# Kernel optimization log

Hardware: AMD Instinct MI355X
Metric: run time of the kernel (lower is better)

The kernel has to match this reference:

```python
import jax, jax.numpy as jnp
import numpy as np

B, N, D, A = 128, 512, 300, 32


def setup_inputs() -> dict:
    key = jax.random.key(0)
    k1, k2, k3, k4 = jax.random.split(key, 4)
    node_reprs = jax.random.normal(k1, (B, N, D), dtype=jnp.float32)
    adjacency_matrices = (jax.random.uniform(k2, (B, N, N)) < 0.1).astype(jnp.float32)
    Wq = jax.random.normal(k3, (D, A), dtype=jnp.float32) * 0.01
    Wk = jax.random.normal(k4, (D, A), dtype=jnp.float32) * 0.01
    return {"node_reprs": node_reprs, "adjacency_matrices": adjacency_matrices,
            "Wq": Wq, "Wk": Wk}


def reference(node_reprs, adjacency_matrices, Wq, Wk):
    # Q = X Wq, K = X Wk  -> [B, N, A]
    Q = jnp.einsum('bnd,da->bna', node_reprs, Wq)
    K = jnp.einsum('bmd,da->bma', node_reprs, Wk)
    # scores elementwise-weighted by adjacency (NOT -inf masking), per original
    QK = jnp.einsum('bna,bma->bnm', Q, K) * adjacency_matrices
    attn = jax.nn.softmax(QK, axis=-1)  # torch softmax(dim=1) on [N,N] = last dim
    # aggregate node representations: [B, N, N] @ [B, N, D]
    return jnp.einsum('bnm,bmd->bnd', attn, node_reprs)
```

## Files before the change

### kernel.cpp

```cpp
#include <hip/hip_runtime.h>
#include <math.h>

constexpr int Bq = 128;
constexpr int Nn = 512;
constexpr int Dd = 300;
constexpr int Aa = 32;
constexpr int DT = 304;

typedef __attribute__((ext_vector_type(8))) short short8;
typedef __attribute__((ext_vector_type(4))) float float4v;

static __device__ __forceinline__ ushort f2bf(float x) {
    unsigned u = __float_as_uint(x);
    return (ushort)((u + 0x7FFF + ((u >> 16) & 1)) >> 16);
}

constexpr int KB_ROWS = 128;
constexpr int DCHUNK = 100;
constexpr int XS_STRIDE = 102;

__global__ __launch_bounds__(256) void proj_qk(
    const float* __restrict__ X, const float* __restrict__ Wq,
    const float* __restrict__ Wk, ushort* __restrict__ Qo, ushort* __restrict__ Ko,
    ushort* __restrict__ XbfT)
{
    __shared__ float xs[KB_ROWS * XS_STRIDE];
    const int b  = blockIdx.y;
    const int n0 = blockIdx.x * KB_ROWS;
    const int t  = threadIdx.x;
    const int c  = t & 15;
    const int r  = t >> 4;
    const int a4 = c * 4;
    const int rbase = r * 8;
    const float* Wbase = (a4 < Aa) ? (Wq + a4) : (Wk + (a4 - Aa));
    const float* Xb = X + ((size_t)(b * Nn + n0)) * Dd;

    float4 acc[8];
#pragma unroll
    for (int j = 0; j < 8; ++j) acc[j] = make_float4(0.f, 0.f, 0.f, 0.f);

    for (int d0 = 0; d0 < Dd; d0 += DCHUNK) {
        for (int l = t; l < KB_ROWS * (DCHUNK / 2); l += 256) {
            int row = l / (DCHUNK / 2);
            int dd2 = l - row * (DCHUNK / 2);
            *(float2*)(xs + row * XS_STRIDE + dd2 * 2) =
                *(const float2*)(Xb + (size_t)row * Dd + d0 + dd2 * 2);
        }
        __syncthreads();
        for (int dd = 0; dd < DCHUNK; ++dd) {
            float4 w4 = *(const float4*)(Wbase + (size_t)(d0 + dd) * Aa);
#pragma unroll
            for (int j = 0; j < 8; ++j) {
                float xv = xs[(rbase + j) * XS_STRIDE + dd];
                acc[j].x += xv * w4.x; acc[j].y += xv * w4.y;
                acc[j].z += xv * w4.z; acc[j].w += xv * w4.w;
            }
        }
        for (int l = t; l < KB_ROWS * DCHUNK; l += 256) {
            int dd  = l >> 7;
            int row = l & 127;
            XbfT[((size_t)b * DT + d0 + dd) * Nn + n0 + row] =
                f2bf(xs[row * XS_STRIDE + dd]);
        }
        __syncthreads();
    }

    ushort* Obase = (a4 < Aa) ? (Qo + a4) : (Ko + (a4 - Aa));
#pragma unroll
    for (int j = 0; j < 8; ++j) {
        int n = n0 + rbase + j;
        ushort4 o;
        o.x = f2bf(acc[j].x); o.y = f2bf(acc[j].y);
        o.z = f2bf(acc[j].z); o.w = f2bf(acc[j].w);
        *(ushort4*)(Obase + (size_t)(b * Nn + n) * Aa) = o;
    }
}

constexpr int TN = 32;

__global__ __launch_bounds__(256, 2) void attn_kernel(
    const float* __restrict__ Adj, const ushort* __restrict__ Qbf,
    const ushort* __restrict__ Kbf, const ushort* __restrict__ XbfT,
    float* __restrict__ Out)
{
    __shared__ __align__(16) ushort fragA[2 * 8192];
    __shared__ __align__(16) float wsum[4][TN];

    const int blk  = blockIdx.x;
    const int b    = ((blk >> 7) << 3) | (blk & 7);
    const int n0   = ((blk >> 3) & 15) * TN;

    const int t    = threadIdx.x;
    const int lane = t & 63;
    const int wv   = t >> 6;
    const int dl   = lane & 15;
    const int quad = lane >> 4;

    short8 qfr[2];
#pragma unroll
    for (int rs = 0; rs < 2; ++rs)
        qfr[rs] = *(const short8*)(Qbf + ((size_t)(b * Nn + n0 + rs * 16 + dl)) * Aa + quad * 8);

    const ushort* Kb    = Kbf + (size_t)b * Nn * Aa + (size_t)dl * Aa + quad * 8;
    const float*  arow0 = Adj + ((size_t)b * Nn + n0 + dl) * Nn + quad * 4;

    float dsum[2] = {0.f, 0.f};
    ushort* wpb = fragA + (quad >> 1) * 128 + dl * 8 + (quad & 1) * 4;

#pragma unroll
    for (int i = 0; i < 4; ++i) {
        const int ks = wv + i * 4;
        const int m0 = ks * 32;
        short8 kf0 = *(const short8*)(Kb + (size_t)m0 * Aa);
        short8 kf1 = *(const short8*)(Kb + (size_t)(m0 + 16) * Aa);
        ushort* wp = wpb + ks * 512;
#pragma unroll
        for (int rs = 0; rs < 2; ++rs) {
            const float* ar = arow0 + (size_t)rs * 16 * Nn + m0;
            float4 a0 = *(const float4*)(ar);
            float4 a1 = *(const float4*)(ar + 16);
            float4v z = {0.f, 0.f, 0.f, 0.f};
            float4v s0 = __builtin_amdgcn_mfma_f32_16x16x32_bf16(kf0, qfr[rs], z, 0, 0, 0);
            float4v s1 = __builtin_amdgcn_mfma_f32_16x16x32_bf16(kf1, qfr[rs], z, 0, 0, 0);
            float e0 = (a0.x != 0.f) ? __expf(s0[0]) : 1.0f;
            float e1 = (a0.y != 0.f) ? __expf(s0[1]) : 1.0f;
            float e2 = (a0.z != 0.f) ? __expf(s0[2]) : 1.0f;
            float e3 = (a0.w != 0.f) ? __expf(s0[3]) : 1.0f;
            float e4 = (a1.x != 0.f) ? __expf(s1[0]) : 1.0f;
            float e5 = (a1.y != 0.f) ? __expf(s1[1]) : 1.0f;
            float e6 = (a1.z != 0.f) ? __expf(s1[2]) : 1.0f;
            float e7 = (a1.w != 0.f) ? __expf(s1[3]) : 1.0f;
            dsum[rs] += ((e0 + e1) + (e2 + e3)) + ((e4 + e5) + (e6 + e7));
            uint2 w0, w1;
            w0.x = (unsigned)f2bf(e0) | ((unsigned)f2bf(e1) << 16);
            w0.y = (unsigned)f2bf(e2) | ((unsigned)f2bf(e3) << 16);
            w1.x = (unsigned)f2bf(e4) | ((unsigned)f2bf(e5) << 16);
            w1.y = (unsigned)f2bf(e6) | ((unsigned)f2bf(e7) << 16);
            *(uint2*)(wp + rs * 8192)       = w0;
            *(uint2*)(wp + rs * 8192 + 256) = w1;
        }
    }

#pragma unroll
    for (int rs = 0; rs < 2; ++rs) {
        float v = dsum[rs];
        v += __shfl_xor(v, 16);
        v += __shfl_xor(v, 32);
        if (lane < 16) wsum[wv][rs * 16 + lane] = v;
    }
    __syncthreads();

    float invr0[4], invr1[4];
    {
        float4 s0 = *(const float4*)&wsum[0][quad * 4];
        float4 s1 = *(const float4*)&wsum[0][16 + quad * 4];
#pragma unroll
        for (int w = 1; w < 4; ++w) {
            float4 t0 = *(const float4*)&wsum[w][quad * 4];
            float4 t1 = *(const float4*)&wsum[w][16 + quad * 4];
            s0.x += t0.x; s0.y += t0.y; s0.z += t0.z; s0.w += t0.w;
            s1.x += t1.x; s1.y += t1.y; s1.z += t1.z; s1.w += t1.w;
        }
        invr0[0] = 1.0f / s0.x; invr0[1] = 1.0f / s0.y;
        invr0[2] = 1.0f / s0.z; invr0[3] = 1.0f / s0.w;
        invr1[0] = 1.0f / s1.x; invr1[1] = 1.0f / s1.y;
        invr1[2] = 1.0f / s1.z; invr1[3] = 1.0f / s1.w;
    }

    const ushort* Xb  = XbfT + ((size_t)b * DT) * Nn;
    const ushort* afp = fragA + (size_t)lane * 8;

    for (int p = 0; p < 3; ++p) {
        const int dta = wv + p * 8;
        if (dta >= DT / 16) break;
        const int dtb = dta + 4;
        if (dtb < DT / 16) {
            const ushort* bba = Xb + (size_t)(dta * 16 + dl) * Nn + quad * 8;
            const ushort* bbb = Xb + (size_t)(dtb * 16 + dl) * Nn + quad * 8;
            float4v a0a = {0.f, 0.f, 0.f, 0.f};
            float4v a1a = {0.f, 0.f, 0.f, 0.f};
            float4v a0b = {0.f, 0.f, 0.f, 0.f};
            float4v a1b = {0.f, 0.f, 0.f, 0.f};
#pragma unroll
            for (int ks = 0; ks < 16; ++ks) {
                short8 bfa = *(const short8*)(bba + ks * 32);
                short8 bfb = *(const short8*)(bbb + ks * 32);
                short8 p0  = *(const short8*)(afp + ks * 512);
                short8 p1  = *(const short8*)(afp + 8192 + ks * 512);
                a0a = __builtin_amdgcn_mfma_f32_16x16x32_bf16(p0, bfa, a0a, 0, 0, 0);
                a1a = __builtin_amdgcn_mfma_f32_16x16x32_bf16(p1, bfa, a1a, 0, 0, 0);
                a0b = __builtin_amdgcn_mfma_f32_16x16x32_bf16(p0, bfb, a0b, 0, 0, 0);
                a1b = __builtin_amdgcn_mfma_f32_16x16x32_bf16(p1, bfb, a1b, 0, 0, 0);
            }
            const int da = dta * 16 + dl;
            const int db = dtb * 16 + dl;
#pragma unroll
            for (int r = 0; r < 4; ++r) {
                float* o0 = Out + ((size_t)(b * Nn + n0 + quad * 4 + r)) * Dd;
                float* o1 = Out + ((size_t)(b * Nn + n0 + 16 + quad * 4 + r)) * Dd;
                o0[da] = a0a[r] * invr0[r];
                o1[da] = a1a[r] * invr1[r];
                o0[db] = a0b[r] * invr0[r];
                o1[db] = a1b[r] * invr1[r];
            }
        } else {
            const ushort* bb = Xb + (size_t)(dta * 16 + dl) * Nn + quad * 8;
            float4v acc0 = {0.f, 0.f, 0.f, 0.f};
            float4v acc1 = {0.f, 0.f, 0.f, 0.f};
#pragma unroll
            for (int ks = 0; ks < 16; ++ks) {
                short8 bf = *(const short8*)(bb + ks * 32);
                short8 p0 = *(const short8*)(afp + ks * 512);
                short8 p1 = *(const short8*)(afp + 8192 + ks * 512);
                acc0 = __builtin_amdgcn_mfma_f32_16x16x32_bf16(p0, bf, acc0, 0, 0, 0);
                acc1 = __builtin_amdgcn_mfma_f32_16x16x32_bf16(p1, bf, acc1, 0, 0, 0);
            }
            const int d = dta * 16 + dl;
            if (d < Dd) {
#pragma unroll
                for (int r = 0; r < 4; ++r) {
                    Out[((size_t)(b * Nn + n0 + quad * 4 + r)) * Dd + d]      = acc0[r] * invr0[r];
                    Out[((size_t)(b * Nn + n0 + 16 + quad * 4 + r)) * Dd + d] = acc1[r] * invr1[r];
                }
            }
        }
    }
}

extern "C" void kernel_launch(void* const* d_in, const int* in_sizes, int n_in,
                              void* d_out, int out_size, void* d_ws, size_t ws_size,
                              hipStream_t stream) {
    const float* X   = (const float*)d_in[0];
    const float* Adj = (const float*)d_in[1];
    const float* Wq  = (const float*)d_in[2];
    const float* Wk  = (const float*)d_in[3];
    float* Out = (float*)d_out;

    ushort* Qbf  = (ushort*)d_ws;
    ushort* Kbf  = (ushort*)((char*)d_ws + (size_t)4 * 1024 * 1024);
    ushort* XbfT = (ushort*)((char*)d_ws + (size_t)8 * 1024 * 1024);

    proj_qk<<<dim3(Nn / KB_ROWS, Bq), 256, 0, stream>>>(X, Wq, Wk, Qbf, Kbf, XbfT);
    attn_kernel<<<dim3(Bq * Nn / TN), 256, 0, stream>>>(Adj, Qbf, Kbf, XbfT, Out);
}
```

Baseline: 407.2 us.

## Hoist K/adjacency loads and software-pipeline X fragment loads in aggregation loop

All K fragments and adjacency float4 values are loaded up front, before the score/exp loop, so their global latency overlaps instead of serializing per iteration. The aggregation phase is restructured so each wave handles five D-tiles in a single unrolled k-loop. X fragments are double-buffered two steps ahead, so MFMA work overlaps global loads. Wave 3 redundantly computes an extra tile (dt 15) that it discards, and register pressure rises from holding 16 float4 plus many short8 buffers, which may reduce occupancy.

```diff
diff --git a/kernel.cpp b/kernel.cpp
--- a/kernel.cpp
+++ b/kernel.cpp
@@ -104,24 +104,39 @@
     const ushort* Kb    = Kbf + (size_t)b * Nn * Aa + (size_t)dl * Aa + quad * 8;
     const float*  arow0 = Adj + ((size_t)b * Nn + n0 + dl) * Nn + quad * 4;
 
+    short8 kfr[8];
+#pragma unroll
+    for (int i = 0; i < 4; ++i) {
+        const int m0 = (wv + i * 4) * 32;
+        kfr[i * 2]     = *(const short8*)(Kb + (size_t)m0 * Aa);
+        kfr[i * 2 + 1] = *(const short8*)(Kb + (size_t)(m0 + 16) * Aa);
+    }
+    float4 ad[16];
+#pragma unroll
+    for (int i = 0; i < 4; ++i) {
+        const int m0 = (wv + i * 4) * 32;
+#pragma unroll
+        for (int rs = 0; rs < 2; ++rs) {
+            const float* ar = arow0 + (size_t)rs * 16 * Nn + m0;
+            ad[i * 4 + rs * 2]     = *(const float4*)(ar);
+            ad[i * 4 + rs * 2 + 1] = *(const float4*)(ar + 16);
+        }
+    }
+
     float dsum[2] = {0.f, 0.f};
     ushort* wpb = fragA + (quad >> 1) * 128 + dl * 8 + (quad & 1) * 4;
 
 #pragma unroll
     for (int i = 0; i < 4; ++i) {
         const int ks = wv + i * 4;
-        const int m0 = ks * 32;
-        short8 kf0 = *(const short8*)(Kb + (size_t)m0 * Aa);
-        short8 kf1 = *(const short8*)(Kb + (size_t)(m0 + 16) * Aa);
         ushort* wp = wpb + ks * 512;
 #pragma unroll
         for (int rs = 0; rs < 2; ++rs) {
-            const float* ar = arow0 + (size_t)rs * 16 * Nn + m0;
-            float4 a0 = *(const float4*)(ar);
-            float4 a1 = *(const float4*)(ar + 16);
+            float4 a0 = ad[i * 4 + rs * 2];
+            float4 a1 = ad[i * 4 + rs * 2 + 1];
             float4v z = {0.f, 0.f, 0.f, 0.f};
-            float4v s0 = __builtin_amdgcn_mfma_f32_16x16x32_bf16(kf0, qfr[rs], z, 0, 0, 0);
-            float4v s1 = __builtin_amdgcn_mfma_f32_16x16x32_bf16(kf1, qfr[rs], z, 0, 0, 0);
+            float4v s0 = __builtin_amdgcn_mfma_f32_16x16x32_bf16(kfr[i * 2],     qfr[rs], z, 0, 0, 0);
+            float4v s1 = __builtin_amdgcn_mfma_f32_16x16x32_bf16(kfr[i * 2 + 1], qfr[rs], z, 0, 0, 0);
             float e0 = (a0.x != 0.f) ? __expf(s0[0]) : 1.0f;
             float e1 = (a0.y != 0.f) ? __expf(s0[1]) : 1.0f;
             float e2 = (a0.z != 0.f) ? __expf(s0[2]) : 1.0f;
@@ -169,59 +184,59 @@
 
     const ushort* Xb  = XbfT + ((size_t)b * DT) * Nn;
     const ushort* afp = fragA + (size_t)lane * 8;
-
-    for (int p = 0; p < 3; ++p) {
-        const int dta = wv + p * 8;
-        if (dta >= DT / 16) break;
-        const int dtb = dta + 4;
-        if (dtb < DT / 16) {
-            const ushort* bba = Xb + (size_t)(dta * 16 + dl) * Nn + quad * 8;
-            const ushort* bbb = Xb + (size_t)(dtb * 16 + dl) * Nn + quad * 8;
-            float4v a0a = {0.f, 0.f, 0.f, 0.f};
-            float4v a1a = {0.f, 0.f, 0.f, 0.f};
-            float4v a0b = {0.f, 0.f, 0.f, 0.f};
-            float4v a1b = {0.f, 0.f, 0.f, 0.f};
-#pragma unroll
-            for (int ks = 0; ks < 16; ++ks) {
-                short8 bfa = *(const short8*)(bba + ks * 32);
-                short8 bfb = *(const short8*)(bbb + ks * 32);
-                short8 p0  = *(const short8*)(afp + ks * 512);
-                short8 p1  = *(const short8*)(afp + 8192 + ks * 512);
-                a0a = __builtin_amdgcn_mfma_f32_16x16x32_bf16(p0, bfa, a0a, 0, 0, 0);
-                a1a = __builtin_amdgcn_mfma_f32_16x16x32_bf16(p1, bfa, a1a, 0, 0, 0);
-                a0b = __builtin_amdgcn_mfma_f32_16x16x32_bf16(p0, bfb, a0b, 0, 0, 0);
-                a1b = __builtin_amdgcn_mfma_f32_16x16x32_bf16(p1, bfb, a1b, 0, 0, 0);
-            }
-            const int da = dta * 16 + dl;
-            const int db = dtb * 16 + dl;
+    const int dt4 = (wv < 3) ? (16 + wv) : 15;
+
+    const ushort* bp[5];
+#pragma unroll
+    for (int i = 0; i < 4; ++i)
+        bp[i] = Xb + (size_t)((wv + i * 4) * 16 + dl) * Nn + quad * 8;
+    bp[4] = Xb + (size_t)(dt4 * 16 + dl) * Nn + quad * 8;
+
+    float4v acc[5][2];
+#pragma unroll
+    for (int i = 0; i < 5; ++i) {
+        acc[i][0] = (float4v){0.f, 0.f, 0.f, 0.f};
+        acc[i][1] = (float4v){0.f, 0.f, 0.f, 0.f};
+    }
+
+    short8 xcur[5], xnxt[5];
+#pragma unroll
+    for (int i = 0; i < 5; ++i) xcur[i] = *(const short8*)(bp[i]);
+#pragma unroll
+    for (int i = 0; i < 5; ++i) xnxt[i] = *(const short8*)(bp[i] + 32);
+
+#pragma unroll
+    for (int ks = 0; ks < 16; ++ks) {
+        short8 p0 = *(const short8*)(afp + ks * 512);
+        short8 p1 = *(const short8*)(afp + 8192 + ks * 512);
+        short8 xc[5];
+#pragma unroll
+        for (int i = 0; i < 5; ++i) xc[i] = xcur[i];
+#pragma unroll
+        for (int i = 0; i < 5; ++i) xcur[i] = xnxt[i];
+        if (ks < 14) {
+#pragma unroll
+            for (int i = 0; i < 5; ++i) xnxt[i] = *(const short8*)(bp[i] + (ks + 2) * 32);
+        }
+#pragma unroll
+        for (int i = 0; i < 5; ++i) {
+            acc[i][0] = __builtin_amdgcn_mfma_f32_16x16x32_bf16(p0, xc[i], acc[i][0], 0, 0, 0);
+            acc[i][1] = __builtin_amdgcn_mfma_f32_16x16x32_bf16(p1, xc[i], acc[i][1], 0, 0, 0);
+        }
+    }
+
+#pragma unroll
+    for (int i = 0; i < 5; ++i) {
+        const int dt = (i < 4) ? (wv + i * 4) : dt4;
+        const int d  = dt * 16 + dl;
+        const bool ok = (i < 4) ? true : (wv < 3 && d < Dd);
+        if (ok) {
 #pragma unroll
             for (int r = 0; r < 4; ++r) {
                 float* o0 = Out + ((size_t)(b * Nn + n0 + quad * 4 + r)) * Dd;
                 float* o1 = Out + ((size_t)(b * Nn + n0 + 16 + quad * 4 + r)) * Dd;
-                o0[da] = a0a[r] * invr0[r];
-                o1[da] = a1a[r] * invr1[r];
-                o0[db] = a0b[r] * invr0[r];
-                o1[db] = a1b[r] * invr1[r];
-            }
-        } else {
-            const ushort* bb = Xb + (size_t)(dta * 16 + dl) * Nn + quad * 8;
-            float4v acc0 = {0.f, 0.f, 0.f, 0.f};
-            float4v acc1 = {0.f, 0.f, 0.f, 0.f};
-#pragma unroll
-            for (int ks = 0; ks < 16; ++ks) {
-                short8 bf = *(const short8*)(bb + ks * 32);
-                short8 p0 = *(const short8*)(afp + ks * 512);
-                short8 p1 = *(const short8*)(afp + 8192 + ks * 512);
-                acc0 = __builtin_amdgcn_mfma_f32_16x16x32_bf16(p0, bf, acc0, 0, 0, 0);
-                acc1 = __builtin_amdgcn_mfma_f32_16x16x32_bf16(p1, bf, acc1, 0, 0, 0);
-            }
-            const int d = dta * 16 + dl;
-            if (d < Dd) {
-#pragma unroll
-                for (int r = 0; r < 4; ++r) {
-                    Out[((size_t)(b * Nn + n0 + quad * 4 + r)) * Dd + d]      = acc0[r] * invr0[r];
-                    Out[((size_t)(b * Nn + n0 + 16 + quad * 4 + r)) * Dd + d] = acc1[r] * invr1[r];
-                }
+                o0[d] = acc[i][0][r] * invr0[r];
+                o1[d] = acc[i][1][r] * invr1[r];
             }
         }
     }
```

New measurement: 416.8 us. +2.4%, slower.

## Compute Q/K projection with bf16 MFMA and vectorize transposed X store

Applied to the files above, without the earlier changes.

Rewrites the projection kernel so X is converted to bf16 in shared memory in 64-wide d chunks, and Wq/Wk are staged transposed in LDS as bf16. Q and K are then computed with 16x16x32 bf16 MFMA instructions instead of scalar FP32 FMAs. The transposed bf16 X copy is written as 8-element vector stores instead of scalar ushort stores. This lowers projection precision to bf16 inputs, which was already the storage format for Q and K.

```diff
diff --git a/kernel.cpp b/kernel.cpp
--- a/kernel.cpp
+++ b/kernel.cpp
@@ -14,65 +14,90 @@
     unsigned u = __float_as_uint(x);
     return (ushort)((u + 0x7FFF + ((u >> 16) & 1)) >> 16);
 }
-
-constexpr int KB_ROWS = 128;
-constexpr int DCHUNK = 100;
-constexpr int XS_STRIDE = 102;
+static __device__ __forceinline__ unsigned pack2(float lo, float hi) {
+    return (unsigned)f2bf(lo) | ((unsigned)f2bf(hi) << 16);
+}
+
+constexpr int PB_ROWS = 128;
+constexpr int WK   = 320;
+constexpr int WSTR = 328;
+constexpr int XSTR = 72;
 
 __global__ __launch_bounds__(256) void proj_qk(
     const float* __restrict__ X, const float* __restrict__ Wq,
     const float* __restrict__ Wk, ushort* __restrict__ Qo, ushort* __restrict__ Ko,
     ushort* __restrict__ XbfT)
 {
-    __shared__ float xs[KB_ROWS * XS_STRIDE];
+    __shared__ __align__(16) ushort wl[64 * WSTR];
+    __shared__ __align__(16) ushort xs[PB_ROWS * XSTR];
+
     const int b  = blockIdx.y;
-    const int n0 = blockIdx.x * KB_ROWS;
-    const int t  = threadIdx.x;
-    const int c  = t & 15;
-    const int r  = t >> 4;
-    const int a4 = c * 4;
-    const int rbase = r * 8;
-    const float* Wbase = (a4 < Aa) ? (Wq + a4) : (Wk + (a4 - Aa));
+    const int n0 = blockIdx.x * PB_ROWS;
+    const int t    = threadIdx.x;
+    const int lane = t & 63;
+    const int wv   = t >> 6;
+    const int dl   = lane & 15;
+    const int quad = lane >> 4;
+
+    for (int l = t; l < 64 * WK; l += 256) {
+        const int k = l >> 6, col = l & 63;
+        float v = 0.f;
+        if (k < Dd) v = (col < 32) ? Wq[k * 32 + col] : Wk[k * 32 + (col - 32)];
+        wl[col * WSTR + k] = f2bf(v);
+    }
+
     const float* Xb = X + ((size_t)(b * Nn + n0)) * Dd;
-
-    float4 acc[8];
-#pragma unroll
-    for (int j = 0; j < 8; ++j) acc[j] = make_float4(0.f, 0.f, 0.f, 0.f);
-
-    for (int d0 = 0; d0 < Dd; d0 += DCHUNK) {
-        for (int l = t; l < KB_ROWS * (DCHUNK / 2); l += 256) {
-            int row = l / (DCHUNK / 2);
-            int dd2 = l - row * (DCHUNK / 2);
-            *(float2*)(xs + row * XS_STRIDE + dd2 * 2) =
-                *(const float2*)(Xb + (size_t)row * Dd + d0 + dd2 * 2);
-        }
+    const int colb = wv * 16 + dl;
+
+    float4v acc[8];
+#pragma unroll
+    for (int rt = 0; rt < 8; ++rt) acc[rt] = (float4v){0.f, 0.f, 0.f, 0.f};
+
+    for (int c = 0; c < 5; ++c) {
         __syncthreads();
-        for (int dd = 0; dd < DCHUNK; ++dd) {
-            float4 w4 = *(const float4*)(Wbase + (size_t)(d0 + dd) * Aa);
-#pragma unroll
-            for (int j = 0; j < 8; ++j) {
-                float xv = xs[(rbase + j) * XS_STRIDE + dd];
-                acc[j].x += xv * w4.x; acc[j].y += xv * w4.y;
-                acc[j].z += xv * w4.z; acc[j].w += xv * w4.w;
-            }
-        }
-        for (int l = t; l < KB_ROWS * DCHUNK; l += 256) {
-            int dd  = l >> 7;
-            int row = l & 127;
-            XbfT[((size_t)b * DT + d0 + dd) * Nn + n0 + row] =
-                f2bf(xs[row * XS_STRIDE + dd]);
+        for (int s = t; s < PB_ROWS * 16; s += 256) {
+            const int row = s >> 4, f4 = s & 15;
+            const int d = c * 64 + f4 * 4;
+            float4 v = make_float4(0.f, 0.f, 0.f, 0.f);
+            if (d < Dd) v = *(const float4*)(Xb + (size_t)row * Dd + d);
+            uint2 pk;
+            pk.x = pack2(v.x, v.y);
+            pk.y = pack2(v.z, v.w);
+            *(uint2*)(xs + row * XSTR + f4 * 4) = pk;
         }
         __syncthreads();
-    }
-
-    ushort* Obase = (a4 < Aa) ? (Qo + a4) : (Ko + (a4 - Aa));
-#pragma unroll
-    for (int j = 0; j < 8; ++j) {
-        int n = n0 + rbase + j;
-        ushort4 o;
-        o.x = f2bf(acc[j].x); o.y = f2bf(acc[j].y);
-        o.z = f2bf(acc[j].z); o.w = f2bf(acc[j].w);
-        *(ushort4*)(Obase + (size_t)(b * Nn + n) * Aa) = o;
+
+        for (int s = t; s < 64 * 16; s += 256) {
+            const int dloc = s >> 4, rg = s & 15;
+            const int d = c * 64 + dloc;
+            if (d < Dd) {
+                short8 o;
+#pragma unroll
+                for (int i = 0; i < 8; ++i) o[i] = (short)xs[(rg * 8 + i) * XSTR + dloc];
+                *(short8*)(XbfT + ((size_t)b * DT + d) * Nn + n0 + rg * 8) = o;
+            }
+        }
+
+        short8 bf0 = *(const short8*)(wl + colb * WSTR + c * 64 + quad * 8);
+        short8 bf1 = *(const short8*)(wl + colb * WSTR + c * 64 + 32 + quad * 8);
+#pragma unroll
+        for (int rt = 0; rt < 8; ++rt) {
+            short8 a0 = *(const short8*)(xs + (rt * 16 + dl) * XSTR + quad * 8);
+            short8 a1 = *(const short8*)(xs + (rt * 16 + dl) * XSTR + 32 + quad * 8);
+            acc[rt] = __builtin_amdgcn_mfma_f32_16x16x32_bf16(a0, bf0, acc[rt], 0, 0, 0);
+            acc[rt] = __builtin_amdgcn_mfma_f32_16x16x32_bf16(a1, bf1, acc[rt], 0, 0, 0);
+        }
+    }
+
+    ushort* Obase = (wv < 2) ? Qo : Ko;
+    const int cbase = (wv & 1) * 16 + dl;
+#pragma unroll
+    for (int rt = 0; rt < 8; ++rt) {
+#pragma unroll
+        for (int r = 0; r < 4; ++r) {
+            const int row = n0 + rt * 16 + quad * 4 + r;
+            Obase[((size_t)(b * Nn + row)) * Aa + cbase] = f2bf(acc[rt][r]);
+        }
     }
 }
 
@@ -240,6 +265,6 @@
     ushort* Kbf  = (ushort*)((char*)d_ws + (size_t)4 * 1024 * 1024);
     ushort* XbfT = (ushort*)((char*)d_ws + (size_t)8 * 1024 * 1024);
 
-    proj_qk<<<dim3(Nn / KB_ROWS, Bq), 256, 0, stream>>>(X, Wq, Wk, Qbf, Kbf, XbfT);
+    proj_qk<<<dim3(Nn / PB_ROWS, Bq), 256, 0, stream>>>(X, Wq, Wk, Qbf, Kbf, XbfT);
     attn_kernel<<<dim3(Bq * Nn / TN), 256, 0, stream>>>(Adj, Qbf, Kbf, XbfT, Out);
 }
```

Result: faster. 395.5 us (-2.9%).
